# Kernel optimization log

Hardware: AMD Instinct MI355X
Metric: run time of the kernel (lower is better)

Reference implementation:

```python
import jax, jax.numpy as jnp
import numpy as np


def setup_inputs() -> dict:
    key = jax.random.key(0)
    ks = jax.random.split(key, 9)
    bs, d, K, h = 2048, 128, 256, 256
    s = 0.02  # weight init scale
    return {
        "xhat": jax.random.normal(ks[0], (bs, d), jnp.float32),
        "x": jax.random.normal(ks[1], (bs, d), jnp.float32),
        "codebook": jax.random.normal(ks[2], (K, d), jnp.float32),
        "Wc": jax.random.normal(ks[3], (d, 2 * d), jnp.float32) * s,
        "bc": jnp.zeros((d,), jnp.float32),
        "W1_0": jax.random.normal(ks[4], (h, d), jnp.float32) * s,
        "W2_0": jax.random.normal(ks[5], (d, h), jnp.float32) * s,
        "W1_1": jax.random.normal(ks[6], (h, d), jnp.float32) * s,
        "W2_1": jax.random.normal(ks[7], (d, h), jnp.float32) * s,
    }


def reference(xhat, x, codebook, Wc, bc, W1_0, W2_0, W1_1, W2_1):
    # QINCoStep.encode: evaluate all K codebook candidates per batch element.
    d = xhat.shape[1]
    # MLPconcat on concat([zqs, xhat], -1): split Wc [d, 2d] into codebook and xhat parts,
    # so we never materialize the (bs*K, 2d) concatenated tensor.
    Wz, Wx = Wc[:, :d], Wc[:, d:]
    z = (codebook + codebook @ Wz.T)[None, :, :] + (xhat @ Wx.T)[:, None, :] + bc  # [bs, K, d]
    for W1, W2 in ((W1_0, W2_0), (W1_1, W2_1)):
        z = z + jax.nn.relu(jnp.einsum("bkd,hd->bkh", z, W1)) @ W2.T
    cand = z + xhat[:, None, :]  # [bs, K, d] candidate reconstructions
    dist = jnp.sum(jnp.square(cand - x[:, None, :]), axis=-1)  # [bs, K]
    codes = jnp.argmin(dist, axis=1)  # [bs]
    xhat_next = jnp.take_along_axis(cand, codes[:, None, None], axis=1)[:, 0]  # [bs, d]
    return codes, xhat_next - xhat
```

## Files before the change

kernel.cpp:

```cpp
#include <hip/hip_runtime.h>


typedef short bf8_t __attribute__((ext_vector_type(8)));
typedef float f32x16 __attribute__((ext_vector_type(16)));

__device__ inline unsigned short f2bh(float x) {
    unsigned u = __float_as_uint(x);
    u += 0x7fffu + ((u >> 16) & 1u);
    return (unsigned short)(u >> 16);
}
__device__ inline float bh2f(unsigned short h) {
    return __uint_as_float(((unsigned)h) << 16);
}
__device__ inline f32x16 mfma_bf(uint4 a, uint4 b, f32x16 c) {
    bf8_t av = __builtin_bit_cast(bf8_t, a);
    bf8_t bv = __builtin_bit_cast(bf8_t, b);
    return __builtin_amdgcn_mfma_f32_32x32x16_bf16(av, bv, c, 0, 0, 0);
}
__device__ inline unsigned addrelu2(unsigned hv, unsigned uv) {
    float h0 = __uint_as_float(hv << 16), h1 = __uint_as_float(hv & 0xFFFF0000u);
    float u0 = __uint_as_float(uv << 16), u1 = __uint_as_float(uv & 0xFFFF0000u);
    float v0 = fmaxf(h0 + u0, 0.f), v1 = fmaxf(h1 + u1, 0.f);
    return ((unsigned)f2bh(v1) << 16) | (unsigned)f2bh(v0);
}
__device__ inline unsigned pack2(float a, float b) {
    return ((unsigned)f2bh(b) << 16) | (unsigned)f2bh(a);
}

#define DELTA 4.0f


__global__ __launch_bounds__(256) void k_transpose(
    const float* __restrict__ Wc,
    const float* __restrict__ W1a, const float* __restrict__ W2a,
    const float* __restrict__ W1b, const float* __restrict__ W2b,
    float* __restrict__ WzT, float* __restrict__ WxT,
    float* __restrict__ W1Ta, float* __restrict__ W2Ta,
    float* __restrict__ W1Tb, float* __restrict__ W2Tb)
{
    int g = blockIdx.x * 256 + threadIdx.x;
    if (g < 16384) {
        int j = g >> 7, d = g & 127;
        WzT[g] = Wc[d * 256 + j];
    } else if (g < 32768) {
        int e = g - 16384; int j = e >> 7, d = e & 127;
        WxT[e] = Wc[d * 256 + 128 + j];
    } else if (g < 65536) {
        int e = g - 32768; int d = e >> 8, h = e & 255;
        W1Ta[e] = W1a[h * 128 + d];
    } else if (g < 98304) {
        int e = g - 65536; int h = e >> 7, i = e & 127;
        W2Ta[e] = W2a[i * 256 + h];
    } else if (g < 131072) {
        int e = g - 98304; int d = e >> 8, h = e & 255;
        W1Tb[e] = W1b[h * 128 + d];
    } else if (g < 163840) {
        int e = g - 131072; int h = e >> 7, i = e & 127;
        W2Tb[e] = W2b[i * 256 + h];
    }
}

__global__ __launch_bounds__(256) void k_pack(
    const float* __restrict__ W2a, const float* __restrict__ W1b,
    const float* __restrict__ W2b, uint4* __restrict__ F)
{
    int idx = blockIdx.x * 256 + threadIdx.x;
    int mat = idx >> 12, fp = idx & 4095;
    int tile = fp >> 6, lane = fp & 63;
    const float* src;
    if (mat == 1) {
        int mt = tile >> 3, kt = tile & 7;
        src = W1b + (32 * mt + (lane & 31)) * 128 + 16 * kt + 8 * (lane >> 5);
    } else {
        const float* W = (mat == 0) ? W2a : W2b;
        int mt = tile >> 4, kt = tile & 15;
        src = W + (32 * mt + (lane & 31)) * 256 + 16 * kt + 8 * (lane >> 5);
    }
    unsigned short hs[8];
#pragma unroll
    for (int j = 0; j < 8; ++j) hs[j] = f2bh(src[j]);
    uint4 hv;
    hv.x = (unsigned)hs[0] | ((unsigned)hs[1] << 16);
    hv.y = (unsigned)hs[2] | ((unsigned)hs[3] << 16);
    hv.z = (unsigned)hs[4] | ((unsigned)hs[5] << 16);
    hv.w = (unsigned)hs[6] | ((unsigned)hs[7] << 16);
    F[idx] = hv;
}

__global__ __launch_bounds__(256) void k_z0(
    const float* __restrict__ cb, const float* __restrict__ bc,
    const float* __restrict__ WzT, float* __restrict__ z0,
    unsigned short* __restrict__ z0bf)
{
    int g = blockIdx.x * 256 + threadIdx.x;
    int k = g >> 7, d = g & 127;
    float acc = bc[d] + cb[k * 128 + d];
    for (int j = 0; j < 128; ++j)
        acc = fmaf(cb[k * 128 + j], WzT[j * 128 + d], acc);
    z0[g] = acc;
    z0bf[g] = f2bh(acc);
}

__global__ __launch_bounds__(256) void k_u(
    const float* __restrict__ xhat, const float* __restrict__ WxT,
    float* __restrict__ u, unsigned short* __restrict__ ubf)
{
    int g = blockIdx.x * 256 + threadIdx.x;
    int bl = g >> 7, d = g & 127;
    const float* xr = xhat + bl * 128;
    float acc = 0.f;
    for (int j = 0; j < 128; ++j)
        acc = fmaf(xr[j], WxT[j * 128 + d], acc);
    u[g] = acc;
    ubf[g] = f2bh(acc);
}

__global__ __launch_bounds__(256) void k_prehz(
    const float* __restrict__ z0, const float* __restrict__ W1a,
    unsigned short* __restrict__ H1f)
{
    __shared__ float s[4][128];
    const int t = threadIdx.x;
    const int r0 = blockIdx.x * 4;
#pragma unroll
    for (int e = t; e < 512; e += 256)
        s[e >> 7][e & 127] = z0[(r0 + (e >> 7)) * 128 + (e & 127)];
    __syncthreads();
    float a[4] = {0.f, 0.f, 0.f, 0.f};
    const float* wr = W1a + t * 128;
    for (int i = 0; i < 128; i += 4) {
        float4 w = *(const float4*)(wr + i);
#pragma unroll
        for (int r = 0; r < 4; ++r)
            a[r] = fmaf(s[r][i], w.x, fmaf(s[r][i+1], w.y, fmaf(s[r][i+2], w.z, fmaf(s[r][i+3], w.w, a[r]))));
    }
    const int kt = t >> 4, half = (t >> 3) & 1, j = t & 7;
#pragma unroll
    for (int r = 0; r < 4; ++r) {
        int k = r0 + r; int kg = k >> 5, col = k & 31;
        H1f[((((kg << 4) + kt) << 6) + (half << 5) + col) * 8 + j] = f2bh(a[r]);
    }
}

__global__ __launch_bounds__(256) void k_prehu(
    const float* __restrict__ u, const float* __restrict__ W1a,
    unsigned short* __restrict__ U1bf)
{
    __shared__ float s[4][128];
    const int t = threadIdx.x;
    const int r0 = blockIdx.x * 4;
#pragma unroll
    for (int e = t; e < 512; e += 256)
        s[e >> 7][e & 127] = u[(r0 + (e >> 7)) * 128 + (e & 127)];
    __syncthreads();
    float a[4] = {0.f, 0.f, 0.f, 0.f};
    const float* wr = W1a + t * 128;
    for (int i = 0; i < 128; i += 4) {
        float4 w = *(const float4*)(wr + i);
#pragma unroll
        for (int r = 0; r < 4; ++r)
            a[r] = fmaf(s[r][i], w.x, fmaf(s[r][i+1], w.y, fmaf(s[r][i+2], w.z, fmaf(s[r][i+3], w.w, a[r]))));
    }
#pragma unroll
    for (int r = 0; r < 4; ++r)
        U1bf[(r0 + r) * 256 + t] = f2bh(a[r]);
}

__global__ __launch_bounds__(512, 6) void k_dist_approx(
    const unsigned short* __restrict__ z0bf, const unsigned short* __restrict__ ubf,
    const float* __restrict__ xhat, const float* __restrict__ x,
    const uint4* __restrict__ H1f, const unsigned short* __restrict__ U1bf,
    const uint4* __restrict__ W2f0, const uint4* __restrict__ W1f1,
    const uint4* __restrict__ W2f1, float* __restrict__ dist)
{
    __shared__ uint4 Zf[2048];
    __shared__ uint4 Hf[1024];

    const int t = threadIdx.x;
    const int lane = t & 63, wave = t >> 6;
    const int wm = wave & 3, wn = wave >> 2;
    const int l31 = lane & 31, l5 = lane >> 5;
    const int b = blockIdx.x >> 1, q = blockIdx.x & 1;
    const int k0 = q << 7;

    f32x16 zs[2];
    {
        const unsigned short* ur = ubf + b * 128;
#pragma unroll
        for (int g = 0; g < 2; ++g) {
            const int colw = ((wn << 1) + g) * 32 + l31;
            const unsigned short* zr = z0bf + (k0 + colw) * 128;
#pragma unroll
            for (int rg = 0; rg < 4; ++rg) {
                const int d0 = 32 * wm + 8 * rg + 4 * l5;
                ushort4 a = *(const ushort4*)(zr + d0);
                ushort4 c = *(const ushort4*)(ur + d0);
                zs[g][4*rg+0] = bh2f(a.x) + bh2f(c.x);
                zs[g][4*rg+1] = bh2f(a.y) + bh2f(c.y);
                zs[g][4*rg+2] = bh2f(a.z) + bh2f(c.z);
                zs[g][4*rg+3] = bh2f(a.w) + bh2f(c.w);
            }
        }
    }

#pragma unroll 1
    for (int r = 0; r < 4; ++r) {
        {
            const int kt = 4 * r + wm;
            const uint4 uv = *(const uint4*)(U1bf + b * 256 + kt * 16 + 8 * l5);
#pragma unroll
            for (int gi = 0; gi < 2; ++gi) {
                const int gabs = 2 * wn + gi;
                const int kg = (q << 2) + gabs;
                uint4 hv = H1f[(((kg << 4) + kt) << 6) + lane];
                uint4 o;
                o.x = addrelu2(hv.x, uv.x);
                o.y = addrelu2(hv.y, uv.y);
                o.z = addrelu2(hv.z, uv.z);
                o.w = addrelu2(hv.w, uv.w);
                Hf[((gabs << 2) + wm) * 64 + lane] = o;
            }
        }
        __syncthreads();
#pragma unroll
        for (int ktl = 0; ktl < 4; ++ktl) {
            uint4 ah = W2f0[((wm << 4) + 4 * r + ktl) * 64 + lane];
#pragma unroll
            for (int g = 0; g < 2; ++g) {
                uint4 bv = Hf[((((wn << 1) + g) << 2) + ktl) * 64 + lane];
                zs[g] = mfma_bf(ah, bv, zs[g]);
            }
        }
        __syncthreads();
    }

#pragma unroll
    for (int g = 0; g < 2; ++g) {
        const int gabs = (wn << 1) + g;
#pragma unroll
        for (int rg = 0; rg < 4; ++rg) {
            uint2 hv;
            hv.x = pack2(zs[g][4*rg+0], zs[g][4*rg+1]);
            hv.y = pack2(zs[g][4*rg+2], zs[g][4*rg+3]);
            uint2* zb2 = (uint2*)&Zf[((gabs << 3) + 2 * wm + (rg >> 1)) * 64];
            zb2[(((rg & 1) << 5) + l31) * 2 + l5] = hv;
        }
    }
    __syncthreads();

    const int tile = wave & 1, cg = wave >> 1;
#pragma unroll 1
    for (int c = 0; c < 4; ++c) {
        f32x16 acc;
#pragma unroll
        for (int rr = 0; rr < 16; ++rr) acc[rr] = 0.f;
        const uint4* pw1 = W1f1 + ((2 * c + tile) << 3) * 64;
#pragma unroll
        for (int kt = 0; kt < 8; ++kt) {
            uint4 bv = Zf[((cg << 3) + kt) * 64 + lane];
            uint4 ah = pw1[kt * 64 + lane];
            acc = mfma_bf(ah, bv, acc);
        }
        __syncthreads();
#pragma unroll
        for (int rg = 0; rg < 4; ++rg) {
            float v0 = fmaxf(acc[4*rg+0], 0.f), v1 = fmaxf(acc[4*rg+1], 0.f);
            float v2 = fmaxf(acc[4*rg+2], 0.f), v3 = fmaxf(acc[4*rg+3], 0.f);
            uint2 hv; hv.x = pack2(v0, v1); hv.y = pack2(v2, v3);
            uint2* hb2 = (uint2*)&Hf[((cg << 2) + (tile << 1) + (rg >> 1)) * 64];
            hb2[(((rg & 1) << 5) + l31) * 2 + l5] = hv;
        }
        __syncthreads();
#pragma unroll
        for (int ktl = 0; ktl < 4; ++ktl) {
            uint4 ah = W2f1[((wm << 4) + 4 * c + ktl) * 64 + lane];
#pragma unroll
            for (int g = 0; g < 2; ++g) {
                uint4 bv = Hf[((((wn << 1) + g) << 2) + ktl) * 64 + lane];
                zs[g] = mfma_bf(ah, bv, zs[g]);
            }
        }
    }

    float* red = (float*)Hf;
    __syncthreads();
#pragma unroll
    for (int g = 0; g < 2; ++g) {
        float s = 0.f;
        const int colw = ((wn << 1) + g) * 32 + l31;
#pragma unroll
        for (int rg = 0; rg < 4; ++rg) {
            const int d0 = 32 * wm + 8 * rg + 4 * l5;
            float4 xh = *(const float4*)(xhat + b * 128 + d0);
            float4 xx = *(const float4*)(x + b * 128 + d0);
            float v;
            v = zs[g][4*rg+0] + xh.x - xx.x; s = fmaf(v, v, s);
            v = zs[g][4*rg+1] + xh.y - xx.y; s = fmaf(v, v, s);
            v = zs[g][4*rg+2] + xh.z - xx.z; s = fmaf(v, v, s);
            v = zs[g][4*rg+3] + xh.w - xx.w; s = fmaf(v, v, s);
        }
        s += __shfl_xor(s, 32, 64);
        if (l5 == 0) red[wm * 128 + colw] = s;
    }
    __syncthreads();
    if (t < 128)
        dist[b * 256 + k0 + t] = red[t] + red[128 + t] + red[256 + t] + red[384 + t];
}

__global__ __launch_bounds__(64) void k_select(
    const float* __restrict__ dist, int* __restrict__ cand_k,
    int* __restrict__ cand_cnt, int2* __restrict__ pairs, int* __restrict__ npairs)
{
    __shared__ int sk[8];
    const int b = blockIdx.x, lane = threadIdx.x;
    float v0 = dist[b * 256 + lane];
    float v1 = dist[b * 256 + 64 + lane];
    float v2 = dist[b * 256 + 128 + lane];
    float v3 = dist[b * 256 + 192 + lane];
    float m = fminf(fminf(v0, v1), fminf(v2, v3));
#pragma unroll
    for (int off = 32; off > 0; off >>= 1) m = fminf(m, __shfl_xor(m, off, 64));
    const float thr = m + DELTA;
    const unsigned long long below = (1ull << lane) - 1;
    float vv[4] = {v0, v1, v2, v3};
    int base = 0;
#pragma unroll
    for (int j = 0; j < 4; ++j) {
        bool p = vv[j] <= thr;
        unsigned long long mask = __ballot(p);
        int pos = base + __popcll(mask & below);
        if (p && pos < 8) sk[pos] = 64 * j + lane;
        base += __popcll(mask);
    }
    __syncthreads();
    if (lane == 0) {
        int c = base > 8 ? 8 : base;
        cand_cnt[b] = c;
        int off = atomicAdd(npairs, c);
        for (int s = 0; s < c; ++s) {
            cand_k[b * 8 + s] = sk[s];
            pairs[off + s] = make_int2(b, (sk[s] << 4) | s);
        }
    }
}

__global__ __launch_bounds__(256) void k_exact(
    const float* __restrict__ z0, const float* __restrict__ u,
    const float* __restrict__ xhat, const float* __restrict__ x,
    const int2* __restrict__ pairs, const int* __restrict__ npairs,
    const float* __restrict__ W1Ta, const float* __restrict__ W2Ta,
    const float* __restrict__ W1Tb, const float* __restrict__ W2Tb,
    float* __restrict__ ex_dist)
{
    __shared__ float z8[8][128];
    __shared__ float h8[8][256];
    __shared__ int pb[8], pk[8], psl[8];
    __shared__ int scnt;
    __shared__ float part[8][32];
    const int t = threadIdx.x;
    if (t == 0) {
        int np = *npairs; if (np > 16384) np = 16384;
        int c = np - (int)blockIdx.x * 8;
        scnt = c < 0 ? 0 : (c > 8 ? 8 : c);
    }
    __syncthreads();
    const int cnt = scnt;
    if (cnt == 0) return;
    if (t < 8) {
        int idx = blockIdx.x * 8 + (t < cnt ? t : cnt - 1);
        int2 p = pairs[idx];
        pb[t] = p.x; pk[t] = p.y >> 4; psl[t] = p.y & 15;
    }
    __syncthreads();
#pragma unroll
    for (int n = 0; n < 4; ++n) {
        int e = n * 256 + t; int r = e >> 7, d = e & 127;
        z8[r][d] = z0[pk[r] * 128 + d] + u[pb[r] * 128 + d];
    }
    __syncthreads();
    const float* W1T = W1Ta; const float* W2T = W2Ta;
#pragma unroll 1
    for (int blk = 0; blk < 2; ++blk) {
        float a1[8] = {0.f,0.f,0.f,0.f,0.f,0.f,0.f,0.f};
        for (int d = 0; d < 128; ++d) {
            const float w = W1T[d * 256 + t];
#pragma unroll
            for (int r = 0; r < 8; ++r) a1[r] = fmaf(z8[r][d], w, a1[r]);
        }
#pragma unroll
        for (int r = 0; r < 8; ++r) h8[r][t] = fmaxf(a1[r], 0.f);
        __syncthreads();
        const int ig = t & 127, rg = (t >> 7) * 4;
        float a2[4] = {0.f,0.f,0.f,0.f};
        for (int h = 0; h < 256; ++h) {
            const float w = W2T[h * 128 + ig];
#pragma unroll
            for (int j = 0; j < 4; ++j) a2[j] = fmaf(h8[rg + j][h], w, a2[j]);
        }
        __syncthreads();
#pragma unroll
        for (int j = 0; j < 4; ++j) z8[rg + j][ig] += a2[j];
        __syncthreads();
        W1T = W1Tb; W2T = W2Tb;
    }
    {
        const int r = t >> 5, c = t & 31;
        const int br = pb[r];
        float s = 0.f;
#pragma unroll
        for (int i = 0; i < 4; ++i) {
            int d = c * 4 + i;
            float v = z8[r][d] + xhat[br * 128 + d] - x[br * 128 + d];
            s = fmaf(v, v, s);
        }
        part[r][c] = s;
    }
    __syncthreads();
    if (t < 8 && t < cnt) {
        float s = 0.f;
#pragma unroll
        for (int c2 = 0; c2 < 32; ++c2) s += part[t][c2];
        ex_dist[pb[t] * 8 + psl[t]] = s;
    }
}

__global__ __launch_bounds__(256) void k_pick(
    const int* __restrict__ cand_k, const int* __restrict__ cand_cnt,
    const float* __restrict__ ex_dist, int* __restrict__ codes,
    float* __restrict__ out0)
{
    int b = blockIdx.x * 256 + threadIdx.x;
    int cnt = cand_cnt[b];
    float bv = ex_dist[b * 8]; int bk = cand_k[b * 8];
    for (int s = 1; s < cnt; ++s) {
        float v = ex_dist[b * 8 + s];
        if (v < bv) { bv = v; bk = cand_k[b * 8 + s]; }
    }
    codes[b] = bk;
    out0[b] = (float)bk;
}

__global__ __launch_bounds__(256) void k_final(
    const float* __restrict__ z0, const float* __restrict__ u,
    const int* __restrict__ codes,
    const float* __restrict__ W1Ta, const float* __restrict__ W2Ta,
    const float* __restrict__ W1Tb, const float* __restrict__ W2Tb,
    float* __restrict__ outd)
{
    __shared__ float z8[8][128];
    __shared__ float h8[8][256];
    __shared__ int ci[8];
    const int t = threadIdx.x;
    const int b0 = blockIdx.x * 8;
    if (t < 8) ci[t] = codes[b0 + t];
    __syncthreads();
#pragma unroll
    for (int n = 0; n < 4; ++n) {
        int e = n * 256 + t; int r = e >> 7, d = e & 127;
        z8[r][d] = z0[ci[r] * 128 + d] + u[(b0 + r) * 128 + d];
    }
    __syncthreads();
    const float* W1T = W1Ta; const float* W2T = W2Ta;
#pragma unroll 1
    for (int blk = 0; blk < 2; ++blk) {
        float a1[8] = {0.f,0.f,0.f,0.f,0.f,0.f,0.f,0.f};
        for (int d = 0; d < 128; ++d) {
            const float w = W1T[d * 256 + t];
#pragma unroll
            for (int r = 0; r < 8; ++r) a1[r] = fmaf(z8[r][d], w, a1[r]);
        }
#pragma unroll
        for (int r = 0; r < 8; ++r) h8[r][t] = fmaxf(a1[r], 0.f);
        __syncthreads();
        const int ig = t & 127, rg = (t >> 7) * 4;
        float a2[4] = {0.f,0.f,0.f,0.f};
        for (int h = 0; h < 256; ++h) {
            const float w = W2T[h * 128 + ig];
#pragma unroll
            for (int j = 0; j < 4; ++j) a2[j] = fmaf(h8[rg + j][h], w, a2[j]);
        }
        __syncthreads();
#pragma unroll
        for (int j = 0; j < 4; ++j) z8[rg + j][ig] += a2[j];
        __syncthreads();
        W1T = W1Tb; W2T = W2Tb;
    }
#pragma unroll
    for (int n = 0; n < 4; ++n) {
        int e = n * 256 + t; int r = e >> 7, d = e & 127;
        outd[(b0 + r) * 128 + d] = z8[r][d];
    }
}

extern "C" void kernel_launch(void* const* d_in, const int* in_sizes, int n_in,
                              void* d_out, int out_size, void* d_ws, size_t ws_size,
                              hipStream_t stream) {
    const float* xhat = (const float*)d_in[0];
    const float* x    = (const float*)d_in[1];
    const float* cb   = (const float*)d_in[2];
    const float* Wc   = (const float*)d_in[3];
    const float* bc   = (const float*)d_in[4];
    const float* W1_0 = (const float*)d_in[5];
    const float* W2_0 = (const float*)d_in[6];
    const float* W1_1 = (const float*)d_in[7];
    const float* W2_1 = (const float*)d_in[8];
    float* out = (float*)d_out;
    float* ws  = (float*)d_ws;

    float* WzT   = ws + 0;
    float* WxT   = ws + 16384;
    float* W1T0  = ws + 32768;
    float* W2T0  = ws + 65536;
    float* W1T1  = ws + 98304;
    float* W2T1  = ws + 131072;
    float* z0    = ws + 163840;
    float* u     = ws + 196608;
    float* dist  = ws + 458752;
    unsigned short* z0bf = (unsigned short*)(ws + 983040);
    unsigned short* ubf  = (unsigned short*)(ws + 999424);
    unsigned short* U1bf = (unsigned short*)(ws + 1130496);
    uint4* H1f   = (uint4*)(ws + 1392640);
    uint4* F     = (uint4*)(ws + 1425408);
    const uint4* W2f0 = F;
    const uint4* W1f1 = F + 4096;
    const uint4* W2f1 = F + 8192;
    int*   cand_k   = (int*)(ws + 1474560);
    int*   cand_cnt = (int*)(ws + 1490944);
    float* ex_dist  = ws + 1492992;
    int2*  pairs    = (int2*)(ws + 1509376);
    int*   npairs   = (int*)(ws + 1542144);
    int*   codes    = (int*)(ws + 1542148);

    k_transpose<<<640, 256, 0, stream>>>(Wc, W1_0, W2_0, W1_1, W2_1,
                                         WzT, WxT, W1T0, W2T0, W1T1, W2T1);
    k_pack<<<48, 256, 0, stream>>>(W2_0, W1_1, W2_1, F);
    k_z0<<<128, 256, 0, stream>>>(cb, bc, WzT, z0, z0bf);
    k_u<<<1024, 256, 0, stream>>>(xhat, WxT, u, ubf);
    k_prehz<<<64, 256, 0, stream>>>(z0, W1_0, (unsigned short*)H1f);
    k_prehu<<<512, 256, 0, stream>>>(u, W1_0, U1bf);
    k_dist_approx<<<4096, 512, 0, stream>>>(z0bf, ubf, xhat, x, H1f, U1bf,
                                            W2f0, W1f1, W2f1, dist);
    hipMemsetAsync(npairs, 0, sizeof(int), stream);
    k_select<<<2048, 64, 0, stream>>>(dist, cand_k, cand_cnt, pairs, npairs);
    k_exact<<<2048, 256, 0, stream>>>(z0, u, xhat, x, pairs, npairs,
                                      W1T0, W2T0, W1T1, W2T1, ex_dist);
    k_pick<<<8, 256, 0, stream>>>(cand_k, cand_cnt, ex_dist, codes, out);
    k_final<<<256, 256, 0, stream>>>(z0, u, codes, W1T0, W2T0, W1T1, W2T1, out + 2048);
}
```

Baseline: 347.5 us.

## Fuse prep kernels, merge select into approx-dist kernel, replace pick with atomicMin

Merges the transpose and pack kernels, and fuses the z0/u projections with their W1 pre-multiplication into two prep kernels. Each approx-dist block now handles all 256 codes for one batch row, so the threshold candidate selection runs in-block and the dist buffer and select kernel go away. The exact stage picks the winner per batch with a packed 64-bit atomicMin, which removes the pick kernel. Fewer launches and less global traffic, in exchange for doubled shared memory per block and a dropped occupancy hint in the main kernel.

```diff
diff --git a/kernel.cpp b/kernel.cpp
--- a/kernel.cpp
+++ b/kernel.cpp
@@ -29,14 +29,14 @@
 
 #define DELTA 4.0f
 
-
-__global__ __launch_bounds__(256) void k_transpose(
+__global__ __launch_bounds__(256) void k_prep1(
     const float* __restrict__ Wc,
     const float* __restrict__ W1a, const float* __restrict__ W2a,
     const float* __restrict__ W1b, const float* __restrict__ W2b,
     float* __restrict__ WzT, float* __restrict__ WxT,
     float* __restrict__ W1Ta, float* __restrict__ W2Ta,
-    float* __restrict__ W1Tb, float* __restrict__ W2Tb)
+    float* __restrict__ W1Tb, float* __restrict__ W2Tb,
+    uint4* __restrict__ F)
 {
     int g = blockIdx.x * 256 + threadIdx.x;
     if (g < 16384) {
@@ -57,139 +57,138 @@
     } else if (g < 163840) {
         int e = g - 131072; int h = e >> 7, i = e & 127;
         W2Tb[e] = W2b[i * 256 + h];
-    }
-}
-
-__global__ __launch_bounds__(256) void k_pack(
-    const float* __restrict__ W2a, const float* __restrict__ W1b,
-    const float* __restrict__ W2b, uint4* __restrict__ F)
-{
-    int idx = blockIdx.x * 256 + threadIdx.x;
-    int mat = idx >> 12, fp = idx & 4095;
-    int tile = fp >> 6, lane = fp & 63;
-    const float* src;
-    if (mat == 1) {
-        int mt = tile >> 3, kt = tile & 7;
-        src = W1b + (32 * mt + (lane & 31)) * 128 + 16 * kt + 8 * (lane >> 5);
-    } else {
-        const float* W = (mat == 0) ? W2a : W2b;
-        int mt = tile >> 4, kt = tile & 15;
-        src = W + (32 * mt + (lane & 31)) * 256 + 16 * kt + 8 * (lane >> 5);
-    }
-    unsigned short hs[8];
-#pragma unroll
-    for (int j = 0; j < 8; ++j) hs[j] = f2bh(src[j]);
-    uint4 hv;
-    hv.x = (unsigned)hs[0] | ((unsigned)hs[1] << 16);
-    hv.y = (unsigned)hs[2] | ((unsigned)hs[3] << 16);
-    hv.z = (unsigned)hs[4] | ((unsigned)hs[5] << 16);
-    hv.w = (unsigned)hs[6] | ((unsigned)hs[7] << 16);
-    F[idx] = hv;
-}
-
-__global__ __launch_bounds__(256) void k_z0(
+    } else if (g < 176128) {
+        int idx = g - 163840;
+        int mat = idx >> 12, fp = idx & 4095;
+        int tile = fp >> 6, lane = fp & 63;
+        const float* src;
+        if (mat == 1) {
+            int mt = tile >> 3, kt = tile & 7;
+            src = W1b + (32 * mt + (lane & 31)) * 128 + 16 * kt + 8 * (lane >> 5);
+        } else {
+            const float* W = (mat == 0) ? W2a : W2b;
+            int mt = tile >> 4, kt = tile & 15;
+            src = W + (32 * mt + (lane & 31)) * 256 + 16 * kt + 8 * (lane >> 5);
+        }
+        unsigned short hs[8];
+#pragma unroll
+        for (int j = 0; j < 8; ++j) hs[j] = f2bh(src[j]);
+        uint4 hv;
+        hv.x = (unsigned)hs[0] | ((unsigned)hs[1] << 16);
+        hv.y = (unsigned)hs[2] | ((unsigned)hs[3] << 16);
+        hv.z = (unsigned)hs[4] | ((unsigned)hs[5] << 16);
+        hv.w = (unsigned)hs[6] | ((unsigned)hs[7] << 16);
+        F[idx] = hv;
+    }
+}
+
+__global__ __launch_bounds__(256) void k_prep_k(
     const float* __restrict__ cb, const float* __restrict__ bc,
-    const float* __restrict__ WzT, float* __restrict__ z0,
-    unsigned short* __restrict__ z0bf)
-{
-    int g = blockIdx.x * 256 + threadIdx.x;
-    int k = g >> 7, d = g & 127;
-    float acc = bc[d] + cb[k * 128 + d];
-    for (int j = 0; j < 128; ++j)
-        acc = fmaf(cb[k * 128 + j], WzT[j * 128 + d], acc);
-    z0[g] = acc;
-    z0bf[g] = f2bh(acc);
-}
-
-__global__ __launch_bounds__(256) void k_u(
-    const float* __restrict__ xhat, const float* __restrict__ WxT,
-    float* __restrict__ u, unsigned short* __restrict__ ubf)
-{
-    int g = blockIdx.x * 256 + threadIdx.x;
-    int bl = g >> 7, d = g & 127;
-    const float* xr = xhat + bl * 128;
-    float acc = 0.f;
-    for (int j = 0; j < 128; ++j)
-        acc = fmaf(xr[j], WxT[j * 128 + d], acc);
-    u[g] = acc;
-    ubf[g] = f2bh(acc);
-}
-
-__global__ __launch_bounds__(256) void k_prehz(
-    const float* __restrict__ z0, const float* __restrict__ W1a,
+    const float* __restrict__ WzT, const float* __restrict__ W1T0,
+    float* __restrict__ z0, unsigned short* __restrict__ z0bf,
     unsigned short* __restrict__ H1f)
 {
-    __shared__ float s[4][128];
+    __shared__ float clds[4][128];
+    __shared__ float zlds[4][128];
     const int t = threadIdx.x;
     const int r0 = blockIdx.x * 4;
 #pragma unroll
     for (int e = t; e < 512; e += 256)
-        s[e >> 7][e & 127] = z0[(r0 + (e >> 7)) * 128 + (e & 127)];
-    __syncthreads();
-    float a[4] = {0.f, 0.f, 0.f, 0.f};
-    const float* wr = W1a + t * 128;
-    for (int i = 0; i < 128; i += 4) {
-        float4 w = *(const float4*)(wr + i);
-#pragma unroll
-        for (int r = 0; r < 4; ++r)
-            a[r] = fmaf(s[r][i], w.x, fmaf(s[r][i+1], w.y, fmaf(s[r][i+2], w.z, fmaf(s[r][i+3], w.w, a[r]))));
-    }
-    const int kt = t >> 4, half = (t >> 3) & 1, j = t & 7;
-#pragma unroll
-    for (int r = 0; r < 4; ++r) {
-        int k = r0 + r; int kg = k >> 5, col = k & 31;
-        H1f[((((kg << 4) + kt) << 6) + (half << 5) + col) * 8 + j] = f2bh(a[r]);
-    }
-}
-
-__global__ __launch_bounds__(256) void k_prehu(
-    const float* __restrict__ u, const float* __restrict__ W1a,
+        clds[e >> 7][e & 127] = cb[(r0 + (e >> 7)) * 128 + (e & 127)];
+    __syncthreads();
+    {
+        const int d = t & 127, r = t >> 7;
+        float a0 = bc[d] + clds[r][d], a1 = bc[d] + clds[r + 2][d];
+        for (int j = 0; j < 128; ++j) {
+            const float w = WzT[j * 128 + d];
+            a0 = fmaf(clds[r][j], w, a0);
+            a1 = fmaf(clds[r + 2][j], w, a1);
+        }
+        z0[(r0 + r) * 128 + d] = a0;  z0bf[(r0 + r) * 128 + d] = f2bh(a0);
+        z0[(r0 + r + 2) * 128 + d] = a1;  z0bf[(r0 + r + 2) * 128 + d] = f2bh(a1);
+        zlds[r][d] = a0; zlds[r + 2][d] = a1;
+    }
+    __syncthreads();
+    {
+        float a[4] = {0.f, 0.f, 0.f, 0.f};
+        for (int d = 0; d < 128; ++d) {
+            const float w = W1T0[d * 256 + t];
+#pragma unroll
+            for (int r = 0; r < 4; ++r) a[r] = fmaf(zlds[r][d], w, a[r]);
+        }
+        const int kt = t >> 4, half = (t >> 3) & 1, j = t & 7;
+#pragma unroll
+        for (int r = 0; r < 4; ++r) {
+            int k = r0 + r; int kg = k >> 5, col = k & 31;
+            H1f[(((kg * 16 + kt) * 64) + half * 32 + col) * 8 + j] = f2bh(a[r]);
+        }
+    }
+}
+
+__global__ __launch_bounds__(256) void k_prep_b(
+    const float* __restrict__ xhat, const float* __restrict__ WxT,
+    const float* __restrict__ W1T0,
+    float* __restrict__ u, unsigned short* __restrict__ ubf,
     unsigned short* __restrict__ U1bf)
 {
-    __shared__ float s[4][128];
+    __shared__ float xlds[4][128];
+    __shared__ float ulds[4][128];
     const int t = threadIdx.x;
     const int r0 = blockIdx.x * 4;
 #pragma unroll
     for (int e = t; e < 512; e += 256)
-        s[e >> 7][e & 127] = u[(r0 + (e >> 7)) * 128 + (e & 127)];
-    __syncthreads();
-    float a[4] = {0.f, 0.f, 0.f, 0.f};
-    const float* wr = W1a + t * 128;
-    for (int i = 0; i < 128; i += 4) {
-        float4 w = *(const float4*)(wr + i);
+        xlds[e >> 7][e & 127] = xhat[(r0 + (e >> 7)) * 128 + (e & 127)];
+    __syncthreads();
+    {
+        const int d = t & 127, r = t >> 7;
+        float a0 = 0.f, a1 = 0.f;
+        for (int j = 0; j < 128; ++j) {
+            const float w = WxT[j * 128 + d];
+            a0 = fmaf(xlds[r][j], w, a0);
+            a1 = fmaf(xlds[r + 2][j], w, a1);
+        }
+        u[(r0 + r) * 128 + d] = a0;  ubf[(r0 + r) * 128 + d] = f2bh(a0);
+        u[(r0 + r + 2) * 128 + d] = a1;  ubf[(r0 + r + 2) * 128 + d] = f2bh(a1);
+        ulds[r][d] = a0; ulds[r + 2][d] = a1;
+    }
+    __syncthreads();
+    {
+        float a[4] = {0.f, 0.f, 0.f, 0.f};
+        for (int d = 0; d < 128; ++d) {
+            const float w = W1T0[d * 256 + t];
+#pragma unroll
+            for (int r = 0; r < 4; ++r) a[r] = fmaf(ulds[r][d], w, a[r]);
+        }
 #pragma unroll
         for (int r = 0; r < 4; ++r)
-            a[r] = fmaf(s[r][i], w.x, fmaf(s[r][i+1], w.y, fmaf(s[r][i+2], w.z, fmaf(s[r][i+3], w.w, a[r]))));
-    }
-#pragma unroll
-    for (int r = 0; r < 4; ++r)
-        U1bf[(r0 + r) * 256 + t] = f2bh(a[r]);
-}
-
-__global__ __launch_bounds__(512, 6) void k_dist_approx(
+            U1bf[(r0 + r) * 256 + t] = f2bh(a[r]);
+    }
+}
+
+__global__ __launch_bounds__(512) void k_dist_approx(
     const unsigned short* __restrict__ z0bf, const unsigned short* __restrict__ ubf,
     const float* __restrict__ xhat, const float* __restrict__ x,
     const uint4* __restrict__ H1f, const unsigned short* __restrict__ U1bf,
     const uint4* __restrict__ W2f0, const uint4* __restrict__ W1f1,
-    const uint4* __restrict__ W2f1, float* __restrict__ dist)
+    const uint4* __restrict__ W2f1,
+    int* __restrict__ cand_k, int2* __restrict__ pairs, int* __restrict__ npairs)
 {
-    __shared__ uint4 Zf[2048];
-    __shared__ uint4 Hf[1024];
+    __shared__ uint4 Zf[4096];
+    __shared__ uint4 Hf[2048];
 
     const int t = threadIdx.x;
     const int lane = t & 63, wave = t >> 6;
     const int wm = wave & 3, wn = wave >> 2;
     const int l31 = lane & 31, l5 = lane >> 5;
-    const int b = blockIdx.x >> 1, q = blockIdx.x & 1;
-    const int k0 = q << 7;
-
-    f32x16 zs[2];
+    const int b = blockIdx.x;
+
+    f32x16 zs[4];
     {
         const unsigned short* ur = ubf + b * 128;
 #pragma unroll
-        for (int g = 0; g < 2; ++g) {
-            const int colw = ((wn << 1) + g) * 32 + l31;
-            const unsigned short* zr = z0bf + (k0 + colw) * 128;
+        for (int g = 0; g < 4; ++g) {
+            const int col = ((wn << 2) + g) * 32 + l31;
+            const unsigned short* zr = z0bf + col * 128;
 #pragma unroll
             for (int rg = 0; rg < 4; ++rg) {
                 const int d0 = 32 * wm + 8 * rg + 4 * l5;
@@ -209,16 +208,15 @@
             const int kt = 4 * r + wm;
             const uint4 uv = *(const uint4*)(U1bf + b * 256 + kt * 16 + 8 * l5);
 #pragma unroll
-            for (int gi = 0; gi < 2; ++gi) {
-                const int gabs = 2 * wn + gi;
-                const int kg = (q << 2) + gabs;
-                uint4 hv = H1f[(((kg << 4) + kt) << 6) + lane];
+            for (int gi = 0; gi < 4; ++gi) {
+                const int cg = (wn << 2) + gi;
+                uint4 hv = H1f[((cg << 4) + kt) * 64 + lane];
                 uint4 o;
                 o.x = addrelu2(hv.x, uv.x);
                 o.y = addrelu2(hv.y, uv.y);
                 o.z = addrelu2(hv.z, uv.z);
                 o.w = addrelu2(hv.w, uv.w);
-                Hf[((gabs << 2) + wm) * 64 + lane] = o;
+                Hf[((cg << 2) + wm) * 64 + lane] = o;
             }
         }
         __syncthreads();
@@ -226,8 +224,8 @@
         for (int ktl = 0; ktl < 4; ++ktl) {
             uint4 ah = W2f0[((wm << 4) + 4 * r + ktl) * 64 + lane];
 #pragma unroll
-            for (int g = 0; g < 2; ++g) {
-                uint4 bv = Hf[((((wn << 1) + g) << 2) + ktl) * 64 + lane];
+            for (int g = 0; g < 4; ++g) {
+                uint4 bv = Hf[((((wn << 2) + g) << 2) + ktl) * 64 + lane];
                 zs[g] = mfma_bf(ah, bv, zs[g]);
             }
         }
@@ -235,59 +233,68 @@
     }
 
 #pragma unroll
-    for (int g = 0; g < 2; ++g) {
-        const int gabs = (wn << 1) + g;
+    for (int g = 0; g < 4; ++g) {
+        const int cg = (wn << 2) + g;
 #pragma unroll
         for (int rg = 0; rg < 4; ++rg) {
             uint2 hv;
             hv.x = pack2(zs[g][4*rg+0], zs[g][4*rg+1]);
             hv.y = pack2(zs[g][4*rg+2], zs[g][4*rg+3]);
-            uint2* zb2 = (uint2*)&Zf[((gabs << 3) + 2 * wm + (rg >> 1)) * 64];
+            uint2* zb2 = (uint2*)&Zf[((cg << 3) + 2 * wm + (rg >> 1)) * 64];
             zb2[(((rg & 1) << 5) + l31) * 2 + l5] = hv;
         }
     }
     __syncthreads();
 
-    const int tile = wave & 1, cg = wave >> 1;
 #pragma unroll 1
     for (int c = 0; c < 4; ++c) {
-        f32x16 acc;
-#pragma unroll
-        for (int rr = 0; rr < 16; ++rr) acc[rr] = 0.f;
-        const uint4* pw1 = W1f1 + ((2 * c + tile) << 3) * 64;
-#pragma unroll
-        for (int kt = 0; kt < 8; ++kt) {
-            uint4 bv = Zf[((cg << 3) + kt) * 64 + lane];
-            uint4 ah = pw1[kt * 64 + lane];
-            acc = mfma_bf(ah, bv, acc);
+        f32x16 a0, a1;
+#pragma unroll
+        for (int rr = 0; rr < 16; ++rr) { a0[rr] = 0.f; a1[rr] = 0.f; }
+        {
+            const uint4* pw1 = W1f1 + ((2 * c + wn) << 3) * 64;
+#pragma unroll
+            for (int kt = 0; kt < 8; ++kt) {
+                uint4 ah = pw1[kt * 64 + lane];
+                uint4 b0 = Zf[(((2 * wm) << 3) + kt) * 64 + lane];
+                uint4 b1 = Zf[(((2 * wm + 1) << 3) + kt) * 64 + lane];
+                a0 = mfma_bf(ah, b0, a0);
+                a1 = mfma_bf(ah, b1, a1);
+            }
         }
         __syncthreads();
 #pragma unroll
         for (int rg = 0; rg < 4; ++rg) {
-            float v0 = fmaxf(acc[4*rg+0], 0.f), v1 = fmaxf(acc[4*rg+1], 0.f);
-            float v2 = fmaxf(acc[4*rg+2], 0.f), v3 = fmaxf(acc[4*rg+3], 0.f);
-            uint2 hv; hv.x = pack2(v0, v1); hv.y = pack2(v2, v3);
-            uint2* hb2 = (uint2*)&Hf[((cg << 2) + (tile << 1) + (rg >> 1)) * 64];
-            hb2[(((rg & 1) << 5) + l31) * 2 + l5] = hv;
+            const int ktl = (wn << 1) + (rg >> 1);
+            const int sl = (((rg & 1) << 5) + l31) * 2 + l5;
+            uint2 hv;
+            hv.x = pack2(fmaxf(a0[4*rg+0], 0.f), fmaxf(a0[4*rg+1], 0.f));
+            hv.y = pack2(fmaxf(a0[4*rg+2], 0.f), fmaxf(a0[4*rg+3], 0.f));
+            ((uint2*)&Hf[(((2 * wm) << 2) + ktl) * 64])[sl] = hv;
+            hv.x = pack2(fmaxf(a1[4*rg+0], 0.f), fmaxf(a1[4*rg+1], 0.f));
+            hv.y = pack2(fmaxf(a1[4*rg+2], 0.f), fmaxf(a1[4*rg+3], 0.f));
+            ((uint2*)&Hf[(((2 * wm + 1) << 2) + ktl) * 64])[sl] = hv;
         }
         __syncthreads();
 #pragma unroll
         for (int ktl = 0; ktl < 4; ++ktl) {
             uint4 ah = W2f1[((wm << 4) + 4 * c + ktl) * 64 + lane];
 #pragma unroll
-            for (int g = 0; g < 2; ++g) {
-                uint4 bv = Hf[((((wn << 1) + g) << 2) + ktl) * 64 + lane];
+            for (int g = 0; g < 4; ++g) {
+                uint4 bv = Hf[((((wn << 2) + g) << 2) + ktl) * 64 + lane];
                 zs[g] = mfma_bf(ah, bv, zs[g]);
             }
         }
     }
 
-    float* red = (float*)Hf;
-    __syncthreads();
-#pragma unroll
-    for (int g = 0; g < 2; ++g) {
+    float* red   = (float*)Hf;
+    float* sdist = (float*)Hf + 1024;
+    int*   sk    = (int*)((float*)Hf + 1280);
+    __syncthreads();
+#pragma unroll
+    for (int g = 0; g < 4; ++g) {
         float s = 0.f;
-        const int colw = ((wn << 1) + g) * 32 + l31;
+        const int col = ((wn << 2) + g) * 32 + l31;
 #pragma unroll
         for (int rg = 0; rg < 4; ++rg) {
             const int d0 = 32 * wm + 8 * rg + 4 * l5;
@@ -300,46 +307,39 @@
             v = zs[g][4*rg+3] + xh.w - xx.w; s = fmaf(v, v, s);
         }
         s += __shfl_xor(s, 32, 64);
-        if (l5 == 0) red[wm * 128 + colw] = s;
-    }
-    __syncthreads();
-    if (t < 128)
-        dist[b * 256 + k0 + t] = red[t] + red[128 + t] + red[256 + t] + red[384 + t];
-}
-
-__global__ __launch_bounds__(64) void k_select(
-    const float* __restrict__ dist, int* __restrict__ cand_k,
-    int* __restrict__ cand_cnt, int2* __restrict__ pairs, int* __restrict__ npairs)
-{
-    __shared__ int sk[8];
-    const int b = blockIdx.x, lane = threadIdx.x;
-    float v0 = dist[b * 256 + lane];
-    float v1 = dist[b * 256 + 64 + lane];
-    float v2 = dist[b * 256 + 128 + lane];
-    float v3 = dist[b * 256 + 192 + lane];
-    float m = fminf(fminf(v0, v1), fminf(v2, v3));
-#pragma unroll
-    for (int off = 32; off > 0; off >>= 1) m = fminf(m, __shfl_xor(m, off, 64));
-    const float thr = m + DELTA;
-    const unsigned long long below = (1ull << lane) - 1;
-    float vv[4] = {v0, v1, v2, v3};
+        if (l5 == 0) red[wm * 256 + col] = s;
+    }
+    __syncthreads();
+    if (t < 256)
+        sdist[t] = red[t] + red[256 + t] + red[512 + t] + red[768 + t];
+    __syncthreads();
     int base = 0;
-#pragma unroll
-    for (int j = 0; j < 4; ++j) {
-        bool p = vv[j] <= thr;
-        unsigned long long mask = __ballot(p);
-        int pos = base + __popcll(mask & below);
-        if (p && pos < 8) sk[pos] = 64 * j + lane;
-        base += __popcll(mask);
-    }
-    __syncthreads();
-    if (lane == 0) {
+    if (wave == 0) {
+        float v[4];
+#pragma unroll
+        for (int j = 0; j < 4; ++j) v[j] = sdist[lane + 64 * j];
+        float m = fminf(fminf(v[0], v[1]), fminf(v[2], v[3]));
+#pragma unroll
+        for (int off = 32; off > 0; off >>= 1) m = fminf(m, __shfl_xor(m, off, 64));
+        const float thr = m + DELTA;
+        const unsigned long long below = (1ull << lane) - 1;
+#pragma unroll
+        for (int j = 0; j < 4; ++j) {
+            bool p = v[j] <= thr;
+            unsigned long long mask = __ballot(p);
+            int pos = base + __popcll(mask & below);
+            if (p && pos < 8) sk[pos] = 64 * j + lane;
+            base += __popcll(mask);
+        }
+    }
+    __syncthreads();
+    if (t == 0) {
         int c = base > 8 ? 8 : base;
-        cand_cnt[b] = c;
         int off = atomicAdd(npairs, c);
         for (int s = 0; s < c; ++s) {
-            cand_k[b * 8 + s] = sk[s];
-            pairs[off + s] = make_int2(b, (sk[s] << 4) | s);
+            int kk = sk[s];
+            cand_k[b * 8 + s] = kk;
+            pairs[off + s] = make_int2(b, (kk << 4) | s);
         }
     }
 }
@@ -350,7 +350,7 @@
     const int2* __restrict__ pairs, const int* __restrict__ npairs,
     const float* __restrict__ W1Ta, const float* __restrict__ W2Ta,
     const float* __restrict__ W1Tb, const float* __restrict__ W2Tb,
-    float* __restrict__ ex_dist)
+    unsigned long long* __restrict__ packed)
 {
     __shared__ float z8[8][128];
     __shared__ float h8[8][256];
@@ -420,39 +420,30 @@
         float s = 0.f;
 #pragma unroll
         for (int c2 = 0; c2 < 32; ++c2) s += part[t][c2];
-        ex_dist[pb[t] * 8 + psl[t]] = s;
-    }
-}
-
-__global__ __launch_bounds__(256) void k_pick(
-    const int* __restrict__ cand_k, const int* __restrict__ cand_cnt,
-    const float* __restrict__ ex_dist, int* __restrict__ codes,
-    float* __restrict__ out0)
-{
-    int b = blockIdx.x * 256 + threadIdx.x;
-    int cnt = cand_cnt[b];
-    float bv = ex_dist[b * 8]; int bk = cand_k[b * 8];
-    for (int s = 1; s < cnt; ++s) {
-        float v = ex_dist[b * 8 + s];
-        if (v < bv) { bv = v; bk = cand_k[b * 8 + s]; }
-    }
-    codes[b] = bk;
-    out0[b] = (float)bk;
+        unsigned long long pk64 = (((unsigned long long)__float_as_uint(s)) << 8)
+                                | (unsigned long long)psl[t];
+        atomicMin(&packed[pb[t]], pk64);
+    }
 }
 
 __global__ __launch_bounds__(256) void k_final(
     const float* __restrict__ z0, const float* __restrict__ u,
-    const int* __restrict__ codes,
+    const unsigned long long* __restrict__ packed, const int* __restrict__ cand_k,
     const float* __restrict__ W1Ta, const float* __restrict__ W2Ta,
     const float* __restrict__ W1Tb, const float* __restrict__ W2Tb,
-    float* __restrict__ outd)
+    float* __restrict__ out0, float* __restrict__ outd)
 {
     __shared__ float z8[8][128];
     __shared__ float h8[8][256];
     __shared__ int ci[8];
     const int t = threadIdx.x;
     const int b0 = blockIdx.x * 8;
-    if (t < 8) ci[t] = codes[b0 + t];
+    if (t < 8) {
+        int slot = (int)(packed[b0 + t] & 0xFFull);
+        int code = cand_k[(b0 + t) * 8 + slot];
+        ci[t] = code;
+        out0[b0 + t] = (float)code;
+    }
     __syncthreads();
 #pragma unroll
     for (int n = 0; n < 4; ++n) {
@@ -515,35 +506,30 @@
     float* W2T1  = ws + 131072;
     float* z0    = ws + 163840;
     float* u     = ws + 196608;
-    float* dist  = ws + 458752;
-    unsigned short* z0bf = (unsigned short*)(ws + 983040);
-    unsigned short* ubf  = (unsigned short*)(ws + 999424);
-    unsigned short* U1bf = (unsigned short*)(ws + 1130496);
-    uint4* H1f   = (uint4*)(ws + 1392640);
-    uint4* F     = (uint4*)(ws + 1425408);
+    unsigned short* z0bf = (unsigned short*)(ws + 458752);
+    unsigned short* ubf  = (unsigned short*)(ws + 475136);
+    unsigned short* U1bf = (unsigned short*)(ws + 606208);
+    unsigned short* H1f  = (unsigned short*)(ws + 868352);
+    uint4* F     = (uint4*)(ws + 901120);
     const uint4* W2f0 = F;
     const uint4* W1f1 = F + 4096;
     const uint4* W2f1 = F + 8192;
-    int*   cand_k   = (int*)(ws + 1474560);
-    int*   cand_cnt = (int*)(ws + 1490944);
-    float* ex_dist  = ws + 1492992;
-    int2*  pairs    = (int2*)(ws + 1509376);
-    int*   npairs   = (int*)(ws + 1542144);
-    int*   codes    = (int*)(ws + 1542148);
-
-    k_transpose<<<640, 256, 0, stream>>>(Wc, W1_0, W2_0, W1_1, W2_1,
-                                         WzT, WxT, W1T0, W2T0, W1T1, W2T1);
-    k_pack<<<48, 256, 0, stream>>>(W2_0, W1_1, W2_1, F);
-    k_z0<<<128, 256, 0, stream>>>(cb, bc, WzT, z0, z0bf);
-    k_u<<<1024, 256, 0, stream>>>(xhat, WxT, u, ubf);
-    k_prehz<<<64, 256, 0, stream>>>(z0, W1_0, (unsigned short*)H1f);
-    k_prehu<<<512, 256, 0, stream>>>(u, W1_0, U1bf);
-    k_dist_approx<<<4096, 512, 0, stream>>>(z0bf, ubf, xhat, x, H1f, U1bf,
-                                            W2f0, W1f1, W2f1, dist);
-    hipMemsetAsync(npairs, 0, sizeof(int), stream);
-    k_select<<<2048, 64, 0, stream>>>(dist, cand_k, cand_cnt, pairs, npairs);
+    int*   cand_k = (int*)(ws + 950272);
+    int2*  pairs  = (int2*)(ws + 966656);
+    int*   npairs = (int*)(ws + 999424);
+    unsigned long long* packed = (unsigned long long*)(ws + 999428);
+
+    k_prep1<<<688, 256, 0, stream>>>(Wc, W1_0, W2_0, W1_1, W2_1,
+                                     WzT, WxT, W1T0, W2T0, W1T1, W2T1, F);
+    k_prep_k<<<64, 256, 0, stream>>>(cb, bc, WzT, W1T0, z0, z0bf, H1f);
+    k_prep_b<<<512, 256, 0, stream>>>(xhat, WxT, W1T0, u, ubf, U1bf);
+    hipMemsetAsync(npairs, 0, 4, stream);
+    hipMemsetAsync(packed, 0xFF, 2048 * 8, stream);
+    k_dist_approx<<<2048, 512, 0, stream>>>(z0bf, ubf, xhat, x, (const uint4*)H1f,
+                                            U1bf, W2f0, W1f1, W2f1,
+                                            cand_k, pairs, npairs);
     k_exact<<<2048, 256, 0, stream>>>(z0, u, xhat, x, pairs, npairs,
-                                      W1T0, W2T0, W1T1, W2T1, ex_dist);
-    k_pick<<<8, 256, 0, stream>>>(cand_k, cand_cnt, ex_dist, codes, out);
-    k_final<<<256, 256, 0, stream>>>(z0, u, codes, W1T0, W2T0, W1T1, W2T1, out + 2048);
-}
+                                      W1T0, W2T0, W1T1, W2T1, packed);
+    k_final<<<256, 256, 0, stream>>>(z0, u, packed, cand_k,
+                                     W1T0, W2T0, W1T1, W2T1, out, out + 2048);
+}
```

New measurement: 348.2 us. About the same (+0.2%).
